# Optimization experiments

Measured on AMD Instinct MI355X. Metric: run time of the kernel, lower is better.

## Reference

```python
import jax, jax.numpy as jnp
import numpy as np

ENC_H = 128
DEC_H = 256
DEC_STEPS = 10


def _gru_cell(x, h, Wih, Whh, bih, bhh):
    # PyTorch GRU cell, gate order (r, z, n)
    gi = x @ Wih.T + bih          # (B, 3H)
    gh = h @ Whh.T + bhh          # (B, 3H)
    H = h.shape[-1]
    ir, iz, inn = gi[:, :H], gi[:, H:2 * H], gi[:, 2 * H:]
    hr, hz, hn = gh[:, :H], gh[:, H:2 * H], gh[:, 2 * H:]
    r = jax.nn.sigmoid(ir + hr)
    z = jax.nn.sigmoid(iz + hz)
    n = jnp.tanh(inn + r * hn)
    return (1.0 - z) * n + z * h


def setup_inputs() -> dict:
    key = jax.random.key(0)
    ks = jax.random.split(key, 12)
    B, S = 4096, 128
    s = 0.1
    return {
        "x": jax.random.normal(ks[0], (B, S, 5), jnp.float32),
        "y": jax.random.normal(ks[1], (B, S, 1), jnp.float32),
        "enc_Wih": jax.random.normal(ks[2], (3 * ENC_H, 5), jnp.float32) * s,
        "enc_Whh": jax.random.normal(ks[3], (3 * ENC_H, ENC_H), jnp.float32) * s,
        "enc_bih": jax.random.normal(ks[4], (3 * ENC_H,), jnp.float32) * s,
        "enc_bhh": jax.random.normal(ks[5], (3 * ENC_H,), jnp.float32) * s,
        "dec_Wih": jax.random.normal(ks[6], (3 * DEC_H, ENC_H + 1), jnp.float32) * s,
        "dec_Whh": jax.random.normal(ks[7], (3 * DEC_H, DEC_H), jnp.float32) * s,
        "dec_bih": jax.random.normal(ks[8], (3 * DEC_H,), jnp.float32) * s,
        "dec_bhh": jax.random.normal(ks[9], (3 * DEC_H,), jnp.float32) * s,
        "lin_W": jax.random.normal(ks[10], (4, DEC_H), jnp.float32) * s,
        "lin_b": jax.random.normal(ks[11], (4,), jnp.float32) * s,
    }


def reference(x, y, enc_Wih, enc_Whh, enc_bih, enc_bhh,
              dec_Wih, dec_Whh, dec_bih, dec_bhh, lin_W, lin_b):
    B, S, _ = x.shape
    xs = jnp.transpose(x, (1, 0, 2))   # (S, B, 5)
    ys = jnp.transpose(y, (1, 0, 2))   # (S, B, 1)

    # Encoder: only the final hidden state (contex) is consumed downstream.
    h0 = jnp.zeros((B, ENC_H), x.dtype)

    def enc_step(h, xt):
        return _gru_cell(xt, h, enc_Wih, enc_Whh, enc_bih, enc_bhh), None

    contex, _ = jax.lax.scan(enc_step, h0, xs)   # (B, 128)

    # Decoder: initial hidden is ones (torch.ones_like(shape)), 10 steps.
    hdec0 = jnp.ones((B, DEC_H), x.dtype)

    def dec_step(h, yt):
        xt = jnp.concatenate([contex, yt], axis=-1)   # (B, 129)
        h2 = _gru_cell(xt, h, dec_Wih, dec_Whh, dec_bih, dec_bhh)
        out = h2 @ lin_W.T + lin_b                    # (B, 4)
        return h2, out

    _, outs = jax.lax.scan(dec_step, hdec0, ys[:DEC_STEPS])  # (10, B, 4)

    # res starts as ones; only first 10 rows written.
    res = jnp.ones((S, B, 4), x.dtype).at[:DEC_STEPS].set(outs)
    return jnp.transpose(res, (1, 0, 2))   # (B, S, 4)
```

## Files before the change

kernel.cpp:

```cpp
#include <hip/hip_runtime.h>

#define B_SZ 4096
#define S_SZ 128
#define XD 5
#define EH 128
#define DH 256
#define DSTEPS 10

typedef short v8s __attribute__((ext_vector_type(8)));
typedef float v4f __attribute__((ext_vector_type(4)));

__device__ __forceinline__ float bf2f(unsigned short u) {
    union { unsigned int i; float f; } v; v.i = ((unsigned int)u) << 16; return v.f;
}
__device__ __forceinline__ unsigned short f2bf(float f) {
    union { float f; unsigned int i; } v; v.f = f;
    unsigned int x = v.i;
    return (unsigned short)((x + 0x7FFFu + ((x >> 16) & 1u)) >> 16);
}
__device__ __forceinline__ float fexp2(float x) { return __builtin_amdgcn_exp2f(x); }
__device__ __forceinline__ float frcp(float x) { return __builtin_amdgcn_rcpf(x); }
__device__ __forceinline__ unsigned int cvt2bf(float lo, float hi) {
    unsigned int r;
    asm("v_cvt_pk_bf16_f32 %0, %1, %2" : "=v"(r) : "v"(lo), "v"(hi));
    return r;
}

#define SC_S (-1.44269504088896f)
#define SC_T ( 2.88539008177793f)

__global__ __launch_bounds__(512) void enc_kernel(
    const float* __restrict__ x,
    const float* __restrict__ Wih32,
    const float* __restrict__ Whh32,
    const float* __restrict__ bih,
    const float* __restrict__ bhh,
    const float* __restrict__ dWih,
    const float* __restrict__ dWhh,
    unsigned short* __restrict__ wihp,
    unsigned short* __restrict__ dWhh_bf,
    unsigned short* __restrict__ ctex)
{
    __shared__ unsigned short xs[S_SZ][16][8];
    __shared__ unsigned short hb[2][16][136];
    __shared__ __align__(16) unsigned short zpad[8];

    const int tid = threadIdx.x;
    const int bid = blockIdx.x;
    const int wv = tid >> 6;
    const int lane = tid & 63;
    const int n = lane & 15;
    const int kg = lane >> 4;
    const int r0 = bid * 16;

    for (int i = bid * 512 + tid; i < 768 * 256; i += 131072) {
        const float sc = ((i >> 8) < 512) ? SC_S : SC_T;
        dWhh_bf[i] = f2bf(sc * dWhh[i]);
    }
    for (int i = bid * 512 + tid; i < 768 * 136; i += 131072) {
        int col = i / 136, k = i - col * 136;
        const float sc = (col < 512) ? SC_S : SC_T;
        wihp[i] = (k < 129) ? f2bf(sc * dWih[col * 129 + k]) : (unsigned short)0;
    }

    for (int i = tid; i < 2 * 16 * 136; i += 512) ((unsigned short*)hb)[i] = 0;
    if (tid < 8) zpad[tid] = 0;
    for (int i = tid; i < 16 * S_SZ * 8; i += 512) {
        int m = i >> 10;
        int rem = i & 1023;
        int t = rem >> 3;
        int j = rem & 7;
        unsigned short v = 0;
        if (j < XD) v = f2bf(x[(size_t)(r0 + m) * (S_SZ * XD) + t * XD + j]);
        else if (j == XD) v = 0x3F80;
        xs[t][m][j] = v;
    }

    const int colw = wv * 16 + n;
    v8s fw[3][4];
    v8s fx[3];
    #pragma unroll
    for (int g = 0; g < 3; ++g) {
        const float sc = (g < 2) ? SC_S : SC_T;
        const int gcol = g * EH + colw;
        #pragma unroll
        for (int kt = 0; kt < 4; ++kt) {
            const float* p = &Whh32[(size_t)gcol * EH + kt * 32 + kg * 8];
            float4 lo = *(const float4*)p;
            float4 hi = *(const float4*)(p + 4);
            v8s f;
            f[0] = (short)f2bf(sc * lo.x); f[1] = (short)f2bf(sc * lo.y);
            f[2] = (short)f2bf(sc * lo.z); f[3] = (short)f2bf(sc * lo.w);
            f[4] = (short)f2bf(sc * hi.x); f[5] = (short)f2bf(sc * hi.y);
            f[6] = (short)f2bf(sc * hi.z); f[7] = (short)f2bf(sc * hi.w);
            fw[g][kt] = f;
        }
        v8s t = {0, 0, 0, 0, 0, 0, 0, 0};
        if (kg == 0) {
            const float* p = &Wih32[gcol * XD];
            #pragma unroll
            for (int j = 0; j < XD; ++j) t[j] = (short)f2bf(sc * p[j]);
            float b = (g < 2) ? (sc * (bih[gcol] + bhh[gcol]))
                              : (sc * bih[gcol]);
            t[XD] = (short)f2bf(b);
        }
        fx[g] = t;
    }
    const float bhn = SC_T * bhh[2 * EH + colw];

    const v4f vzero = {0.f, 0.f, 0.f, 0.f};
    float hst[4] = {0.f, 0.f, 0.f, 0.f};
    __syncthreads();

    #pragma unroll 2
    for (int t = 0; t < S_SZ; ++t) {
        const int p = t & 1;
        v8s a[4];
        #pragma unroll
        for (int kt = 0; kt < 4; ++kt)
            a[kt] = *(const v8s*)&hb[p][n][kt * 32 + kg * 8];
        const unsigned short* xsrc = (kg == 0) ? &xs[t][n][0] : &zpad[0];
        v8s ax = *(const v8s*)xsrc;

        v4f accr  = __builtin_amdgcn_mfma_f32_16x16x32_bf16(a[0], fw[0][0], vzero, 0, 0, 0);
        v4f accz  = __builtin_amdgcn_mfma_f32_16x16x32_bf16(a[0], fw[1][0], vzero, 0, 0, 0);
        v4f acchn = __builtin_amdgcn_mfma_f32_16x16x32_bf16(a[0], fw[2][0], vzero, 0, 0, 0);
        #pragma unroll
        for (int kt = 1; kt < 4; ++kt) {
            accr  = __builtin_amdgcn_mfma_f32_16x16x32_bf16(a[kt], fw[0][kt], accr, 0, 0, 0);
            accz  = __builtin_amdgcn_mfma_f32_16x16x32_bf16(a[kt], fw[1][kt], accz, 0, 0, 0);
            acchn = __builtin_amdgcn_mfma_f32_16x16x32_bf16(a[kt], fw[2][kt], acchn, 0, 0, 0);
        }
        accr = __builtin_amdgcn_mfma_f32_16x16x32_bf16(ax, fx[0], accr, 0, 0, 0);
        accz = __builtin_amdgcn_mfma_f32_16x16x32_bf16(ax, fx[1], accz, 0, 0, 0);
        v4f accin = __builtin_amdgcn_mfma_f32_16x16x32_bf16(ax, fx[2], vzero, 0, 0, 0);

        float hnew[4];
        #pragma unroll
        for (int e = 0; e < 4; ++e) {
            float r  = frcp(1.f + fexp2(accr[e]));
            float z  = frcp(1.f + fexp2(accz[e]));
            float nn = 1.f - 2.f * frcp(fexp2(accin[e] + r * (acchn[e] + bhn)) + 1.f);
            float h  = nn + z * (hst[e] - nn);
            hst[e] = h;
            hnew[e] = h;
        }
        const unsigned int pk01 = cvt2bf(hnew[0], hnew[1]);
        const unsigned int pk23 = cvt2bf(hnew[2], hnew[3]);
        hb[1 - p][kg * 4 + 0][colw] = (unsigned short)(pk01 & 0xFFFFu);
        hb[1 - p][kg * 4 + 1][colw] = (unsigned short)(pk01 >> 16);
        hb[1 - p][kg * 4 + 2][colw] = (unsigned short)(pk23 & 0xFFFFu);
        hb[1 - p][kg * 4 + 3][colw] = (unsigned short)(pk23 >> 16);
        __syncthreads();
    }
    #pragma unroll
    for (int e = 0; e < 4; ++e)
        ctex[(size_t)(r0 + kg * 4 + e) * EH + colw] = f2bf(hst[e]);
}

__global__ __launch_bounds__(512, 2)
void dec_all_kernel(
    const unsigned short* __restrict__ dWhh_bf,
    const unsigned short* __restrict__ wihp,
    const float* __restrict__ dbih,
    const float* __restrict__ dbhh,
    const float* __restrict__ y,
    const unsigned short* __restrict__ ctex,
    const float* __restrict__ linW,
    const float* __restrict__ linb,
    float* __restrict__ out)
{
    __shared__ unsigned short hshf[32 * 16 * 8];
    __shared__ unsigned short lwf[32 * 16 * 8];
    __shared__ float gish[512 * 29];
    __shared__ float wysh[512 * 29];
    __shared__ float ysh[16][DSTEPS];

    const int tid  = threadIdx.x;
    const int w    = tid >> 6;
    const int lane = tid & 63;
    const int n    = lane & 15;
    const int kg   = lane >> 4;
    const int rb   = blockIdx.x * 16;
    const int cbase = w * 32;

    {
        int col = tid >> 5, kgrp = tid & 31;
        unsigned short v8[8];
        #pragma unroll
        for (int j = 0; j < 8; ++j)
            v8[j] = (col < 4) ? f2bf(linW[col * 256 + kgrp * 8 + j]) : (unsigned short)0;
        *(uint4*)&lwf[(kgrp * 16 + col) * 8] = *(uint4*)v8;
    }
    if (tid < 16 * DSTEPS) {
        int row = tid / DSTEPS, tt = tid - row * DSTEPS;
        ysh[row][tt] = y[(size_t)(rb + row) * S_SZ + tt];
    }
    for (int i = tid; i < 32 * 16 * 8; i += 512) hshf[i] = 0x3F80;

    v8s fB[3][2][8];
    #pragma unroll
    for (int g = 0; g < 3; ++g)
        #pragma unroll
        for (int cg = 0; cg < 2; ++cg)
            #pragma unroll
            for (int kt = 0; kt < 8; ++kt)
                fB[g][cg][kt] = *(const v8s*)
                    &dWhh_bf[(size_t)(g * DH + cbase + cg * 16 + n) * DH + kt * 32 + kg * 8];

    const v4f vzero = {0.f, 0.f, 0.f, 0.f};
    v4f gi[3][2];
    #pragma unroll
    for (int g = 0; g < 3; ++g)
        #pragma unroll
        for (int cg = 0; cg < 2; ++cg) gi[g][cg] = vzero;

    #pragma unroll
    for (int kt = 0; kt < 4; ++kt) {
        v8s actex = *(const v8s*)&ctex[(size_t)(rb + n) * EH + kt * 32 + kg * 8];
        #pragma unroll
        for (int g = 0; g < 3; ++g)
            #pragma unroll
            for (int cg = 0; cg < 2; ++cg) {
                v8s bw = *(const v8s*)
                    &wihp[(size_t)(g * DH + cbase + cg * 16 + n) * 136 + kt * 32 + kg * 8];
                gi[g][cg] = __builtin_amdgcn_mfma_f32_16x16x32_bf16(bw, actex, gi[g][cg], 0, 0, 0);
            }
    }

    #pragma unroll
    for (int g = 0; g < 3; ++g) {
        const float sc = (g < 2) ? SC_S : SC_T;
        #pragma unroll
        for (int cg = 0; cg < 2; ++cg) {
            #pragma unroll
            for (int e = 0; e < 4; ++e) {
                const int col = cbase + cg * 16 + kg * 4 + e;
                const int gcol = g * DH + col;
                float bb = sc * (dbih[gcol] + ((g < 2) ? dbhh[gcol] : 0.f));
                gi[g][cg][e] += bb;
                wysh[tid * 29 + (g * 2 + cg) * 4 + e] = bf2f(wihp[(size_t)gcol * 136 + 128]);
            }
        }
    }
    #pragma unroll
    for (int g = 0; g < 3; ++g)
        #pragma unroll
        for (int cg = 0; cg < 2; ++cg)
            *(v4f*)&gish[tid * 29 + (g * 2 + cg) * 4] = gi[g][cg];
    #pragma unroll
    for (int e = 0; e < 4; ++e) {
        gish[tid * 29 + 24 + e] = SC_T * dbhh[2 * DH + cbase + 0 * 16 + kg * 4 + e];
        wysh[tid * 29 + 24 + e] = SC_T * dbhh[2 * DH + cbase + 1 * 16 + kg * 4 + e];
    }

    const float4 lb4 = *(const float4*)linb;
    float hprev[2][4];
    #pragma unroll
    for (int cg = 0; cg < 2; ++cg)
        #pragma unroll
        for (int e = 0; e < 4; ++e) hprev[cg][e] = 1.0f;

    __syncthreads();

    for (int t = 0; t < DSTEPS; ++t) {
        const float yv = ysh[n][t];

        v4f ar[2], az[2], an[2];
        #pragma unroll
        for (int cg = 0; cg < 2; ++cg) { ar[cg] = vzero; az[cg] = vzero; an[cg] = vzero; }

        #pragma unroll
        for (int kt = 0; kt < 8; ++kt) {
            v8s a = *(const v8s*)&hshf[((kt * 4 + kg) * 16 + n) * 8];
            #pragma unroll
            for (int cg = 0; cg < 2; ++cg) {
                ar[cg] = __builtin_amdgcn_mfma_f32_16x16x32_bf16(fB[0][cg][kt], a, ar[cg], 0, 0, 0);
                az[cg] = __builtin_amdgcn_mfma_f32_16x16x32_bf16(fB[1][cg][kt], a, az[cg], 0, 0, 0);
                an[cg] = __builtin_amdgcn_mfma_f32_16x16x32_bf16(fB[2][cg][kt], a, an[cg], 0, 0, 0);
            }
        }
        __syncthreads();

        #pragma unroll
        for (int cg = 0; cg < 2; ++cg) {
            v4f giR = *(const v4f*)&gish[tid * 29 + (0 * 2 + cg) * 4];
            v4f giZ = *(const v4f*)&gish[tid * 29 + (1 * 2 + cg) * 4];
            v4f giN = *(const v4f*)&gish[tid * 29 + (2 * 2 + cg) * 4];
            v4f wyR = *(const v4f*)&wysh[tid * 29 + (0 * 2 + cg) * 4];
            v4f wyZ = *(const v4f*)&wysh[tid * 29 + (1 * 2 + cg) * 4];
            v4f wyN = *(const v4f*)&wysh[tid * 29 + (2 * 2 + cg) * 4];
            v4f bN  = (cg == 0) ? *(const v4f*)&gish[tid * 29 + 24]
                                : *(const v4f*)&wysh[tid * 29 + 24];
            float hh[4];
            #pragma unroll
            for (int e = 0; e < 4; ++e) {
                float r  = frcp(1.f + fexp2(giR[e] + yv * wyR[e] + ar[cg][e]));
                float z  = frcp(1.f + fexp2(giZ[e] + yv * wyZ[e] + az[cg][e]));
                float nn = 1.f - 2.f * frcp(
                    fexp2(giN[e] + yv * wyN[e] + r * (an[cg][e] + bN[e])) + 1.f);
                float h  = nn + z * (hprev[cg][e] - nn);
                hprev[cg][e] = h;
                hh[e] = h;
            }
            const unsigned int p01 = cvt2bf(hh[0], hh[1]);
            const unsigned int p23 = cvt2bf(hh[2], hh[3]);
            const int base = cbase + cg * 16 + kg * 4;
            const int idx = (((base >> 3) * 16) + n) * 8 + (base & 7);
            *(uint2*)&hshf[idx] = (uint2){p01, p23};
        }
        __syncthreads();

        if (w == (t & 7)) {
            v4f o4 = vzero;
            #pragma unroll
            for (int kt = 0; kt < 8; ++kt) {
                v8s a = *(const v8s*)&hshf[((kt * 4 + kg) * 16 + n) * 8];
                v8s b = *(const v8s*)&lwf[((kt * 4 + kg) * 16 + n) * 8];
                o4 = __builtin_amdgcn_mfma_f32_16x16x32_bf16(b, a, o4, 0, 0, 0);
            }
            if (kg == 0) {
                float4 ov = {o4[0] + lb4.x, o4[1] + lb4.y, o4[2] + lb4.z, o4[3] + lb4.w};
                *(float4*)&out[(size_t)(rb + n) * (S_SZ * 4) + t * 4] = ov;
            }
        }
    }

    for (int j = tid; j < 16 * 512; j += 512) {
        int row = j >> 9, c = j & 511;
        if (c >= DSTEPS * 4) out[(size_t)(rb + row) * 512 + c] = 1.0f;
    }
}

extern "C" void kernel_launch(void* const* d_in, const int* in_sizes, int n_in,
                              void* d_out, int out_size, void* d_ws, size_t ws_size,
                              hipStream_t stream)
{
    const float* x    = (const float*)d_in[0];
    const float* y    = (const float*)d_in[1];
    const float* eWih = (const float*)d_in[2];
    const float* eWhh = (const float*)d_in[3];
    const float* ebih = (const float*)d_in[4];
    const float* ebhh = (const float*)d_in[5];
    const float* dWih = (const float*)d_in[6];
    const float* dWhh = (const float*)d_in[7];
    const float* dbih = (const float*)d_in[8];
    const float* dbhh = (const float*)d_in[9];
    const float* linW = (const float*)d_in[10];
    const float* linb = (const float*)d_in[11];
    float* out = (float*)d_out;

    char* ws = (char*)d_ws;
    unsigned short* wihp    = (unsigned short*)(ws);
    unsigned short* dWhh_bf = (unsigned short*)(ws + 208896);
    unsigned short* ctex    = (unsigned short*)(ws + 602112);

    enc_kernel<<<256, 512, 0, stream>>>(x, eWih, eWhh, ebih, ebhh,
                                        dWih, dWhh, wihp, dWhh_bf, ctex);
    dec_all_kernel<<<256, 512, 0, stream>>>(dWhh_bf, wihp, dbih, dbhh, y,
                                            ctex, linW, linb, out);
}
```

Before: 209.9 us.

## Fuse encoder and decoder into one kernel, split weight prep into own kernel

Merges the encoder GRU and the decoder into a single kernel, so the context vector stays in shared memory (hb[0]) and is no longer written to and read back from global memory. The encoder's x staging buffer and the decoder's gi/wy tables share one shared-memory union. Decoder weight conversion moves into a separate small prep kernel that runs before the fused one. The fused kernel uses more shared memory and registers, and its launch bound is raised to 512 threads with 2 blocks per CU, which may limit occupancy or cause spills in the encoder phase. The launch count stays at two.

New measurement: 235.6 us. 1.12x slower.

```diff
diff --git a/kernel.cpp b/kernel.cpp
--- a/kernel.cpp
+++ b/kernel.cpp
@@ -29,21 +29,46 @@
 #define SC_S (-1.44269504088896f)
 #define SC_T ( 2.88539008177793f)
 
-__global__ __launch_bounds__(512) void enc_kernel(
+__global__ __launch_bounds__(256) void prep_kernel(
+    const float* __restrict__ dWih,
+    const float* __restrict__ dWhh,
+    unsigned short* __restrict__ wihp,
+    unsigned short* __restrict__ dWhh_bf)
+{
+    const int gsz = gridDim.x * 256;
+    for (int i = blockIdx.x * 256 + threadIdx.x; i < 768 * 256; i += gsz) {
+        const float sc = ((i >> 8) < 512) ? SC_S : SC_T;
+        dWhh_bf[i] = f2bf(sc * dWhh[i]);
+    }
+    for (int i = blockIdx.x * 256 + threadIdx.x; i < 768 * 136; i += gsz) {
+        int col = i / 136, k = i - col * 136;
+        const float sc = (col < 512) ? SC_S : SC_T;
+        wihp[i] = (k < 129) ? f2bf(sc * dWih[col * 129 + k]) : (unsigned short)0;
+    }
+}
+
+__global__ __launch_bounds__(512, 2)
+void fused_kernel(
     const float* __restrict__ x,
     const float* __restrict__ Wih32,
     const float* __restrict__ Whh32,
     const float* __restrict__ bih,
     const float* __restrict__ bhh,
-    const float* __restrict__ dWih,
-    const float* __restrict__ dWhh,
-    unsigned short* __restrict__ wihp,
-    unsigned short* __restrict__ dWhh_bf,
-    unsigned short* __restrict__ ctex)
+    const float* __restrict__ dbih,
+    const float* __restrict__ dbhh,
+    const float* __restrict__ y,
+    const unsigned short* __restrict__ wihp,
+    const unsigned short* __restrict__ dWhh_bf,
+    const float* __restrict__ linW,
+    const float* __restrict__ linb,
+    float* __restrict__ out)
 {
-    __shared__ unsigned short xs[S_SZ][16][8];
+    __shared__ __align__(16) char uni[118784];
     __shared__ unsigned short hb[2][16][136];
     __shared__ __align__(16) unsigned short zpad[8];
+    __shared__ unsigned short hshf[32 * 16 * 8];
+    __shared__ unsigned short lwf[32 * 16 * 8];
+    __shared__ float ysh[16][DSTEPS];
 
     const int tid = threadIdx.x;
     const int bid = blockIdx.x;
@@ -53,282 +78,254 @@
     const int kg = lane >> 4;
     const int r0 = bid * 16;
 
-    for (int i = bid * 512 + tid; i < 768 * 256; i += 131072) {
-        const float sc = ((i >> 8) < 512) ? SC_S : SC_T;
-        dWhh_bf[i] = f2bf(sc * dWhh[i]);
+    {
+        auto xs = (unsigned short (*)[16][8])uni;
+
+        for (int i = tid; i < 2 * 16 * 136; i += 512) ((unsigned short*)hb)[i] = 0;
+        if (tid < 8) zpad[tid] = 0;
+        for (int i = tid; i < 16 * S_SZ * 8; i += 512) {
+            int m = i >> 10;
+            int rem = i & 1023;
+            int t = rem >> 3;
+            int j = rem & 7;
+            unsigned short v = 0;
+            if (j < XD) v = f2bf(x[(size_t)(r0 + m) * (S_SZ * XD) + t * XD + j]);
+            else if (j == XD) v = 0x3F80;
+            xs[t][m][j] = v;
+        }
+
+        const int colw = wv * 16 + n;
+        v8s fw[3][4];
+        v8s fx[3];
+        #pragma unroll
+        for (int g = 0; g < 3; ++g) {
+            const float sc = (g < 2) ? SC_S : SC_T;
+            const int gcol = g * EH + colw;
+            #pragma unroll
+            for (int kt = 0; kt < 4; ++kt) {
+                const float* p = &Whh32[(size_t)gcol * EH + kt * 32 + kg * 8];
+                float4 lo = *(const float4*)p;
+                float4 hi = *(const float4*)(p + 4);
+                v8s f;
+                f[0] = (short)f2bf(sc * lo.x); f[1] = (short)f2bf(sc * lo.y);
+                f[2] = (short)f2bf(sc * lo.z); f[3] = (short)f2bf(sc * lo.w);
+                f[4] = (short)f2bf(sc * hi.x); f[5] = (short)f2bf(sc * hi.y);
+                f[6] = (short)f2bf(sc * hi.z); f[7] = (short)f2bf(sc * hi.w);
+                fw[g][kt] = f;
+            }
+            v8s t = {0, 0, 0, 0, 0, 0, 0, 0};
+            if (kg == 0) {
+                const float* p = &Wih32[gcol * XD];
+                #pragma unroll
+                for (int j = 0; j < XD; ++j) t[j] = (short)f2bf(sc * p[j]);
+                float b = (g < 2) ? (sc * (bih[gcol] + bhh[gcol]))
+                                  : (sc * bih[gcol]);
+                t[XD] = (short)f2bf(b);
+            }
+            fx[g] = t;
+        }
+        const float bhn = SC_T * bhh[2 * EH + colw];
+
+        const v4f vzero = {0.f, 0.f, 0.f, 0.f};
+        float hst[4] = {0.f, 0.f, 0.f, 0.f};
+        __syncthreads();
+
+        #pragma unroll 2
+        for (int t = 0; t < S_SZ; ++t) {
+            const int p = t & 1;
+            v8s a[4];
+            #pragma unroll
+            for (int kt = 0; kt < 4; ++kt)
+                a[kt] = *(const v8s*)&hb[p][n][kt * 32 + kg * 8];
+            const unsigned short* xsrc = (kg == 0) ? &xs[t][n][0] : &zpad[0];
+            v8s ax = *(const v8s*)xsrc;
+
+            v4f accr  = __builtin_amdgcn_mfma_f32_16x16x32_bf16(a[0], fw[0][0], vzero, 0, 0, 0);
+            v4f accz  = __builtin_amdgcn_mfma_f32_16x16x32_bf16(a[0], fw[1][0], vzero, 0, 0, 0);
+            v4f acchn = __builtin_amdgcn_mfma_f32_16x16x32_bf16(a[0], fw[2][0], vzero, 0, 0, 0);
+            #pragma unroll
+            for (int kt = 1; kt < 4; ++kt) {
+                accr  = __builtin_amdgcn_mfma_f32_16x16x32_bf16(a[kt], fw[0][kt], accr, 0, 0, 0);
+                accz  = __builtin_amdgcn_mfma_f32_16x16x32_bf16(a[kt], fw[1][kt], accz, 0, 0, 0);
+                acchn = __builtin_amdgcn_mfma_f32_16x16x32_bf16(a[kt], fw[2][kt], acchn, 0, 0, 0);
+            }
+            accr = __builtin_amdgcn_mfma_f32_16x16x32_bf16(ax, fx[0], accr, 0, 0, 0);
+            accz = __builtin_amdgcn_mfma_f32_16x16x32_bf16(ax, fx[1], accz, 0, 0, 0);
+            v4f accin = __builtin_amdgcn_mfma_f32_16x16x32_bf16(ax, fx[2], vzero, 0, 0, 0);
+
+            float hnew[4];
+            #pragma unroll
+            for (int e = 0; e < 4; ++e) {
+                float r  = frcp(1.f + fexp2(accr[e]));
+                float z  = frcp(1.f + fexp2(accz[e]));
+                float nn = 1.f - 2.f * frcp(fexp2(accin[e] + r * (acchn[e] + bhn)) + 1.f);
+                float h  = nn + z * (hst[e] - nn);
+                hst[e] = h;
+                hnew[e] = h;
+            }
+            const unsigned int pk01 = cvt2bf(hnew[0], hnew[1]);
+            const unsigned int pk23 = cvt2bf(hnew[2], hnew[3]);
+            hb[1 - p][kg * 4 + 0][colw] = (unsigned short)(pk01 & 0xFFFFu);
+            hb[1 - p][kg * 4 + 1][colw] = (unsigned short)(pk01 >> 16);
+            hb[1 - p][kg * 4 + 2][colw] = (unsigned short)(pk23 & 0xFFFFu);
+            hb[1 - p][kg * 4 + 3][colw] = (unsigned short)(pk23 >> 16);
+            __syncthreads();
+        }
     }
-    for (int i = bid * 512 + tid; i < 768 * 136; i += 131072) {
-        int col = i / 136, k = i - col * 136;
-        const float sc = (col < 512) ? SC_S : SC_T;
-        wihp[i] = (k < 129) ? f2bf(sc * dWih[col * 129 + k]) : (unsigned short)0;
-    }
-
-    for (int i = tid; i < 2 * 16 * 136; i += 512) ((unsigned short*)hb)[i] = 0;
-    if (tid < 8) zpad[tid] = 0;
-    for (int i = tid; i < 16 * S_SZ * 8; i += 512) {
-        int m = i >> 10;
-        int rem = i & 1023;
-        int t = rem >> 3;
-        int j = rem & 7;
-        unsigned short v = 0;
-        if (j < XD) v = f2bf(x[(size_t)(r0 + m) * (S_SZ * XD) + t * XD + j]);
-        else if (j == XD) v = 0x3F80;
-        xs[t][m][j] = v;
-    }
-
-    const int colw = wv * 16 + n;
-    v8s fw[3][4];
-    v8s fx[3];
-    #pragma unroll
-    for (int g = 0; g < 3; ++g) {
-        const float sc = (g < 2) ? SC_S : SC_T;
-        const int gcol = g * EH + colw;
+
+    {
+        const int w = wv;
+        const int cbase = w * 32;
+        const int rb = r0;
+        float* gish = (float*)uni;
+        float* wysh = (float*)(uni + 59392);
+
+        {
+            int col = tid >> 5, kgrp = tid & 31;
+            unsigned short v8[8];
+            #pragma unroll
+            for (int j = 0; j < 8; ++j)
+                v8[j] = (col < 4) ? f2bf(linW[col * 256 + kgrp * 8 + j]) : (unsigned short)0;
+            *(uint4*)&lwf[(kgrp * 16 + col) * 8] = *(uint4*)v8;
+        }
+        if (tid < 16 * DSTEPS) {
+            int row = tid / DSTEPS, tt = tid - row * DSTEPS;
+            ysh[row][tt] = y[(size_t)(rb + row) * S_SZ + tt];
+        }
+        for (int i = tid; i < 32 * 16 * 8; i += 512) hshf[i] = 0x3F80;
+
+        v8s fB[3][2][8];
+        #pragma unroll
+        for (int g = 0; g < 3; ++g)
+            #pragma unroll
+            for (int cg = 0; cg < 2; ++cg)
+                #pragma unroll
+                for (int kt = 0; kt < 8; ++kt)
+                    fB[g][cg][kt] = *(const v8s*)
+                        &dWhh_bf[(size_t)(g * DH + cbase + cg * 16 + n) * DH + kt * 32 + kg * 8];
+
+        const v4f vzero = {0.f, 0.f, 0.f, 0.f};
+        v4f gi[3][2];
+        #pragma unroll
+        for (int g = 0; g < 3; ++g)
+            #pragma unroll
+            for (int cg = 0; cg < 2; ++cg) gi[g][cg] = vzero;
+
         #pragma unroll
         for (int kt = 0; kt < 4; ++kt) {
-            const float* p = &Whh32[(size_t)gcol * EH + kt * 32 + kg * 8];
-            float4 lo = *(const float4*)p;
-            float4 hi = *(const float4*)(p + 4);
-            v8s f;
-            f[0] = (short)f2bf(sc * lo.x); f[1] = (short)f2bf(sc * lo.y);
-            f[2] = (short)f2bf(sc * lo.z); f[3] = (short)f2bf(sc * lo.w);
-            f[4] = (short)f2bf(sc * hi.x); f[5] = (short)f2bf(sc * hi.y);
-            f[6] = (short)f2bf(sc * hi.z); f[7] = (short)f2bf(sc * hi.w);
-            fw[g][kt] = f;
-        }
-        v8s t = {0, 0, 0, 0, 0, 0, 0, 0};
-        if (kg == 0) {
-            const float* p = &Wih32[gcol * XD];
-            #pragma unroll
-            for (int j = 0; j < XD; ++j) t[j] = (short)f2bf(sc * p[j]);
-            float b = (g < 2) ? (sc * (bih[gcol] + bhh[gcol]))
-                              : (sc * bih[gcol]);
-            t[XD] = (short)f2bf(b);
-        }
-        fx[g] = t;
-    }
-    const float bhn = SC_T * bhh[2 * EH + colw];
-
-    const v4f vzero = {0.f, 0.f, 0.f, 0.f};
-    float hst[4] = {0.f, 0.f, 0.f, 0.f};
-    __syncthreads();
-
-    #pragma unroll 2
-    for (int t = 0; t < S_SZ; ++t) {
-        const int p = t & 1;
-        v8s a[4];
-        #pragma unroll
-        for (int kt = 0; kt < 4; ++kt)
-            a[kt] = *(const v8s*)&hb[p][n][kt * 32 + kg * 8];
-        const unsigned short* xsrc = (kg == 0) ? &xs[t][n][0] : &zpad[0];
-        v8s ax = *(const v8s*)xsrc;
-
-        v4f accr  = __builtin_amdgcn_mfma_f32_16x16x32_bf16(a[0], fw[0][0], vzero, 0, 0, 0);
-        v4f accz  = __builtin_amdgcn_mfma_f32_16x16x32_bf16(a[0], fw[1][0], vzero, 0, 0, 0);
-        v4f acchn = __builtin_amdgcn_mfma_f32_16x16x32_bf16(a[0], fw[2][0], vzero, 0, 0, 0);
-        #pragma unroll
-        for (int kt = 1; kt < 4; ++kt) {
-            accr  = __builtin_amdgcn_mfma_f32_16x16x32_bf16(a[kt], fw[0][kt], accr, 0, 0, 0);
-            accz  = __builtin_amdgcn_mfma_f32_16x16x32_bf16(a[kt], fw[1][kt], accz, 0, 0, 0);
-            acchn = __builtin_amdgcn_mfma_f32_16x16x32_bf16(a[kt], fw[2][kt], acchn, 0, 0, 0);
-        }
-        accr = __builtin_amdgcn_mfma_f32_16x16x32_bf16(ax, fx[0], accr, 0, 0, 0);
-        accz = __builtin_amdgcn_mfma_f32_16x16x32_bf16(ax, fx[1], accz, 0, 0, 0);
-        v4f accin = __builtin_amdgcn_mfma_f32_16x16x32_bf16(ax, fx[2], vzero, 0, 0, 0);
-
-        float hnew[4];
+            v8s actex = *(const v8s*)&hb[0][n][kt * 32 + kg * 8];
+            #pragma unroll
+            for (int g = 0; g < 3; ++g)
+                #pragma unroll
+                for (int cg = 0; cg < 2; ++cg) {
+                    v8s bw = *(const v8s*)
+                        &wihp[(size_t)(g * DH + cbase + cg * 16 + n) * 136 + kt * 32 + kg * 8];
+                    gi[g][cg] = __builtin_amdgcn_mfma_f32_16x16x32_bf16(bw, actex, gi[g][cg], 0, 0, 0);
+                }
+        }
+
+        #pragma unroll
+        for (int g = 0; g < 3; ++g) {
+            const float sc = (g < 2) ? SC_S : SC_T;
+            #pragma unroll
+            for (int cg = 0; cg < 2; ++cg) {
+                #pragma unroll
+                for (int e = 0; e < 4; ++e) {
+                    const int col = cbase + cg * 16 + kg * 4 + e;
+                    const int gcol = g * DH + col;
+                    float bb = sc * (dbih[gcol] + ((g < 2) ? dbhh[gcol] : 0.f));
+                    gi[g][cg][e] += bb;
+                    wysh[tid * 29 + (g * 2 + cg) * 4 + e] = bf2f(wihp[(size_t)gcol * 136 + 128]);
+                }
+            }
+        }
+        #pragma unroll
+        for (int g = 0; g < 3; ++g)
+            #pragma unroll
+            for (int cg = 0; cg < 2; ++cg)
+                *(v4f*)&gish[tid * 29 + (g * 2 + cg) * 4] = gi[g][cg];
         #pragma unroll
         for (int e = 0; e < 4; ++e) {
-            float r  = frcp(1.f + fexp2(accr[e]));
-            float z  = frcp(1.f + fexp2(accz[e]));
-            float nn = 1.f - 2.f * frcp(fexp2(accin[e] + r * (acchn[e] + bhn)) + 1.f);
-            float h  = nn + z * (hst[e] - nn);
-            hst[e] = h;
-            hnew[e] = h;
-        }
-        const unsigned int pk01 = cvt2bf(hnew[0], hnew[1]);
-        const unsigned int pk23 = cvt2bf(hnew[2], hnew[3]);
-        hb[1 - p][kg * 4 + 0][colw] = (unsigned short)(pk01 & 0xFFFFu);
-        hb[1 - p][kg * 4 + 1][colw] = (unsigned short)(pk01 >> 16);
-        hb[1 - p][kg * 4 + 2][colw] = (unsigned short)(pk23 & 0xFFFFu);
-        hb[1 - p][kg * 4 + 3][colw] = (unsigned short)(pk23 >> 16);
+            gish[tid * 29 + 24 + e] = SC_T * dbhh[2 * DH + cbase + 0 * 16 + kg * 4 + e];
+            wysh[tid * 29 + 24 + e] = SC_T * dbhh[2 * DH + cbase + 1 * 16 + kg * 4 + e];
+        }
+
+        const float4 lb4 = *(const float4*)linb;
+        float hprev[2][4];
+        #pragma unroll
+        for (int cg = 0; cg < 2; ++cg)
+            #pragma unroll
+            for (int e = 0; e < 4; ++e) hprev[cg][e] = 1.0f;
+
         __syncthreads();
-    }
-    #pragma unroll
-    for (int e = 0; e < 4; ++e)
-        ctex[(size_t)(r0 + kg * 4 + e) * EH + colw] = f2bf(hst[e]);
-}
-
-__global__ __launch_bounds__(512, 2)
-void dec_all_kernel(
-    const unsigned short* __restrict__ dWhh_bf,
-    const unsigned short* __restrict__ wihp,
-    const float* __restrict__ dbih,
-    const float* __restrict__ dbhh,
-    const float* __restrict__ y,
-    const unsigned short* __restrict__ ctex,
-    const float* __restrict__ linW,
-    const float* __restrict__ linb,
-    float* __restrict__ out)
-{
-    __shared__ unsigned short hshf[32 * 16 * 8];
-    __shared__ unsigned short lwf[32 * 16 * 8];
-    __shared__ float gish[512 * 29];
-    __shared__ float wysh[512 * 29];
-    __shared__ float ysh[16][DSTEPS];
-
-    const int tid  = threadIdx.x;
-    const int w    = tid >> 6;
-    const int lane = tid & 63;
-    const int n    = lane & 15;
-    const int kg   = lane >> 4;
-    const int rb   = blockIdx.x * 16;
-    const int cbase = w * 32;
-
-    {
-        int col = tid >> 5, kgrp = tid & 31;
-        unsigned short v8[8];
-        #pragma unroll
-        for (int j = 0; j < 8; ++j)
-            v8[j] = (col < 4) ? f2bf(linW[col * 256 + kgrp * 8 + j]) : (unsigned short)0;
-        *(uint4*)&lwf[(kgrp * 16 + col) * 8] = *(uint4*)v8;
-    }
-    if (tid < 16 * DSTEPS) {
-        int row = tid / DSTEPS, tt = tid - row * DSTEPS;
-        ysh[row][tt] = y[(size_t)(rb + row) * S_SZ + tt];
-    }
-    for (int i = tid; i < 32 * 16 * 8; i += 512) hshf[i] = 0x3F80;
-
-    v8s fB[3][2][8];
-    #pragma unroll
-    for (int g = 0; g < 3; ++g)
-        #pragma unroll
-        for (int cg = 0; cg < 2; ++cg)
-            #pragma unroll
-            for (int kt = 0; kt < 8; ++kt)
-                fB[g][cg][kt] = *(const v8s*)
-                    &dWhh_bf[(size_t)(g * DH + cbase + cg * 16 + n) * DH + kt * 32 + kg * 8];
-
-    const v4f vzero = {0.f, 0.f, 0.f, 0.f};
-    v4f gi[3][2];
-    #pragma unroll
-    for (int g = 0; g < 3; ++g)
-        #pragma unroll
-        for (int cg = 0; cg < 2; ++cg) gi[g][cg] = vzero;
-
-    #pragma unroll
-    for (int kt = 0; kt < 4; ++kt) {
-        v8s actex = *(const v8s*)&ctex[(size_t)(rb + n) * EH + kt * 32 + kg * 8];
-        #pragma unroll
-        for (int g = 0; g < 3; ++g)
-            #pragma unroll
-            for (int cg = 0; cg < 2; ++cg) {
-                v8s bw = *(const v8s*)
-                    &wihp[(size_t)(g * DH + cbase + cg * 16 + n) * 136 + kt * 32 + kg * 8];
-                gi[g][cg] = __builtin_amdgcn_mfma_f32_16x16x32_bf16(bw, actex, gi[g][cg], 0, 0, 0);
-            }
-    }
-
-    #pragma unroll
-    for (int g = 0; g < 3; ++g) {
-        const float sc = (g < 2) ? SC_S : SC_T;
-        #pragma unroll
-        for (int cg = 0; cg < 2; ++cg) {
-            #pragma unroll
-            for (int e = 0; e < 4; ++e) {
-                const int col = cbase + cg * 16 + kg * 4 + e;
-                const int gcol = g * DH + col;
-                float bb = sc * (dbih[gcol] + ((g < 2) ? dbhh[gcol] : 0.f));
-                gi[g][cg][e] += bb;
-                wysh[tid * 29 + (g * 2 + cg) * 4 + e] = bf2f(wihp[(size_t)gcol * 136 + 128]);
-            }
-        }
-    }
-    #pragma unroll
-    for (int g = 0; g < 3; ++g)
-        #pragma unroll
-        for (int cg = 0; cg < 2; ++cg)
-            *(v4f*)&gish[tid * 29 + (g * 2 + cg) * 4] = gi[g][cg];
-    #pragma unroll
-    for (int e = 0; e < 4; ++e) {
-        gish[tid * 29 + 24 + e] = SC_T * dbhh[2 * DH + cbase + 0 * 16 + kg * 4 + e];
-        wysh[tid * 29 + 24 + e] = SC_T * dbhh[2 * DH + cbase + 1 * 16 + kg * 4 + e];
-    }
-
-    const float4 lb4 = *(const float4*)linb;
-    float hprev[2][4];
-    #pragma unroll
-    for (int cg = 0; cg < 2; ++cg)
-        #pragma unroll
-        for (int e = 0; e < 4; ++e) hprev[cg][e] = 1.0f;
-
-    __syncthreads();
-
-    for (int t = 0; t < DSTEPS; ++t) {
-        const float yv = ysh[n][t];
-
-        v4f ar[2], az[2], an[2];
-        #pragma unroll
-        for (int cg = 0; cg < 2; ++cg) { ar[cg] = vzero; az[cg] = vzero; an[cg] = vzero; }
-
-        #pragma unroll
-        for (int kt = 0; kt < 8; ++kt) {
-            v8s a = *(const v8s*)&hshf[((kt * 4 + kg) * 16 + n) * 8];
-            #pragma unroll
-            for (int cg = 0; cg < 2; ++cg) {
-                ar[cg] = __builtin_amdgcn_mfma_f32_16x16x32_bf16(fB[0][cg][kt], a, ar[cg], 0, 0, 0);
-                az[cg] = __builtin_amdgcn_mfma_f32_16x16x32_bf16(fB[1][cg][kt], a, az[cg], 0, 0, 0);
-                an[cg] = __builtin_amdgcn_mfma_f32_16x16x32_bf16(fB[2][cg][kt], a, an[cg], 0, 0, 0);
-            }
-        }
-        __syncthreads();
-
-        #pragma unroll
-        for (int cg = 0; cg < 2; ++cg) {
-            v4f giR = *(const v4f*)&gish[tid * 29 + (0 * 2 + cg) * 4];
-            v4f giZ = *(const v4f*)&gish[tid * 29 + (1 * 2 + cg) * 4];
-            v4f giN = *(const v4f*)&gish[tid * 29 + (2 * 2 + cg) * 4];
-            v4f wyR = *(const v4f*)&wysh[tid * 29 + (0 * 2 + cg) * 4];
-            v4f wyZ = *(const v4f*)&wysh[tid * 29 + (1 * 2 + cg) * 4];
-            v4f wyN = *(const v4f*)&wysh[tid * 29 + (2 * 2 + cg) * 4];
-            v4f bN  = (cg == 0) ? *(const v4f*)&gish[tid * 29 + 24]
-                                : *(const v4f*)&wysh[tid * 29 + 24];
-            float hh[4];
-            #pragma unroll
-            for (int e = 0; e < 4; ++e) {
-                float r  = frcp(1.f + fexp2(giR[e] + yv * wyR[e] + ar[cg][e]));
-                float z  = frcp(1.f + fexp2(giZ[e] + yv * wyZ[e] + az[cg][e]));
-                float nn = 1.f - 2.f * frcp(
-                    fexp2(giN[e] + yv * wyN[e] + r * (an[cg][e] + bN[e])) + 1.f);
-                float h  = nn + z * (hprev[cg][e] - nn);
-                hprev[cg][e] = h;
-                hh[e] = h;
-            }
-            const unsigned int p01 = cvt2bf(hh[0], hh[1]);
-            const unsigned int p23 = cvt2bf(hh[2], hh[3]);
-            const int base = cbase + cg * 16 + kg * 4;
-            const int idx = (((base >> 3) * 16) + n) * 8 + (base & 7);
-            *(uint2*)&hshf[idx] = (uint2){p01, p23};
-        }
-        __syncthreads();
-
-        if (w == (t & 7)) {
-            v4f o4 = vzero;
+
+        for (int t = 0; t < DSTEPS; ++t) {
+            const float yv = ysh[n][t];
+
+            v4f ar[2], az[2], an[2];
+            #pragma unroll
+            for (int cg = 0; cg < 2; ++cg) { ar[cg] = vzero; az[cg] = vzero; an[cg] = vzero; }
+
             #pragma unroll
             for (int kt = 0; kt < 8; ++kt) {
                 v8s a = *(const v8s*)&hshf[((kt * 4 + kg) * 16 + n) * 8];
-                v8s b = *(const v8s*)&lwf[((kt * 4 + kg) * 16 + n) * 8];
-                o4 = __builtin_amdgcn_mfma_f32_16x16x32_bf16(b, a, o4, 0, 0, 0);
-            }
-            if (kg == 0) {
-                float4 ov = {o4[0] + lb4.x, o4[1] + lb4.y, o4[2] + lb4.z, o4[3] + lb4.w};
-                *(float4*)&out[(size_t)(rb + n) * (S_SZ * 4) + t * 4] = ov;
-            }
-        }
-    }
-
-    for (int j = tid; j < 16 * 512; j += 512) {
-        int row = j >> 9, c = j & 511;
-        if (c >= DSTEPS * 4) out[(size_t)(rb + row) * 512 + c] = 1.0f;
+                #pragma unroll
+                for (int cg = 0; cg < 2; ++cg) {
+                    ar[cg] = __builtin_amdgcn_mfma_f32_16x16x32_bf16(fB[0][cg][kt], a, ar[cg], 0, 0, 0);
+                    az[cg] = __builtin_amdgcn_mfma_f32_16x16x32_bf16(fB[1][cg][kt], a, az[cg], 0, 0, 0);
+                    an[cg] = __builtin_amdgcn_mfma_f32_16x16x32_bf16(fB[2][cg][kt], a, an[cg], 0, 0, 0);
+                }
+            }
+            __syncthreads();
+
+            #pragma unroll
+            for (int cg = 0; cg < 2; ++cg) {
+                v4f giR = *(const v4f*)&gish[tid * 29 + (0 * 2 + cg) * 4];
+                v4f giZ = *(const v4f*)&gish[tid * 29 + (1 * 2 + cg) * 4];
+                v4f giN = *(const v4f*)&gish[tid * 29 + (2 * 2 + cg) * 4];
+                v4f wyR = *(const v4f*)&wysh[tid * 29 + (0 * 2 + cg) * 4];
+                v4f wyZ = *(const v4f*)&wysh[tid * 29 + (1 * 2 + cg) * 4];
+                v4f wyN = *(const v4f*)&wysh[tid * 29 + (2 * 2 + cg) * 4];
+                v4f bN  = (cg == 0) ? *(const v4f*)&gish[tid * 29 + 24]
+                                    : *(const v4f*)&wysh[tid * 29 + 24];
+                float hh[4];
+                #pragma unroll
+                for (int e = 0; e < 4; ++e) {
+                    float r  = frcp(1.f + fexp2(giR[e] + yv * wyR[e] + ar[cg][e]));
+                    float z  = frcp(1.f + fexp2(giZ[e] + yv * wyZ[e] + az[cg][e]));
+                    float nn = 1.f - 2.f * frcp(
+                        fexp2(giN[e] + yv * wyN[e] + r * (an[cg][e] + bN[e])) + 1.f);
+                    float h  = nn + z * (hprev[cg][e] - nn);
+                    hprev[cg][e] = h;
+                    hh[e] = h;
+                }
+                const unsigned int p01 = cvt2bf(hh[0], hh[1]);
+                const unsigned int p23 = cvt2bf(hh[2], hh[3]);
+                const int base = cbase + cg * 16 + kg * 4;
+                const int idx = (((base >> 3) * 16) + n) * 8 + (base & 7);
+                *(uint2*)&hshf[idx] = (uint2){p01, p23};
+            }
+            __syncthreads();
+
+            if (w == (t & 7)) {
+                v4f o4 = vzero;
+                #pragma unroll
+                for (int kt = 0; kt < 8; ++kt) {
+                    v8s a = *(const v8s*)&hshf[((kt * 4 + kg) * 16 + n) * 8];
+                    v8s b = *(const v8s*)&lwf[((kt * 4 + kg) * 16 + n) * 8];
+                    o4 = __builtin_amdgcn_mfma_f32_16x16x32_bf16(b, a, o4, 0, 0, 0);
+                }
+                if (kg == 0) {
+                    float4 ov = {o4[0] + lb4.x, o4[1] + lb4.y, o4[2] + lb4.z, o4[3] + lb4.w};
+                    *(float4*)&out[(size_t)(rb + n) * (S_SZ * 4) + t * 4] = ov;
+                }
+            }
+        }
+
+        for (int j = tid; j < 16 * 512; j += 512) {
+            int row = j >> 9, c = j & 511;
+            if (c >= DSTEPS * 4) out[(size_t)(rb + row) * 512 + c] = 1.0f;
+        }
     }
 }
 
@@ -353,10 +350,9 @@
     char* ws = (char*)d_ws;
     unsigned short* wihp    = (unsigned short*)(ws);
     unsigned short* dWhh_bf = (unsigned short*)(ws + 208896);
-    unsigned short* ctex    = (unsigned short*)(ws + 602112);
-
-    enc_kernel<<<256, 512, 0, stream>>>(x, eWih, eWhh, ebih, ebhh,
-                                        dWih, dWhh, wihp, dWhh_bf, ctex);
-    dec_all_kernel<<<256, 512, 0, stream>>>(dWhh_bf, wihp, dbih, dbhh, y,
-                                            ctex, linW, linb, out);
-}
+
+    prep_kernel<<<256, 256, 0, stream>>>(dWih, dWhh, wihp, dWhh_bf);
+    fused_kernel<<<256, 512, 0, stream>>>(x, eWih, eWhh, ebih, ebhh,
+                                          dbih, dbhh, y, wihp, dWhh_bf,
+                                          linW, linb, out);
+}
```
